# Optimization experiments

Hardware: AMD Instinct MI355X
Metric: run time of the kernel (lower is better)

Reference implementation:

```python
import jax, jax.numpy as jnp
import numpy as np

IN_F = 4096
OUT_F = 4096
N = 16384


def setup_inputs() -> dict:
    key = jax.random.key(0)
    ks = jax.random.split(key, 7)
    return {
        "x": jax.random.normal(ks[0], (N, IN_F), dtype=jnp.float32),
        "weight_mu": jax.random.normal(ks[1], (OUT_F, IN_F), dtype=jnp.float32) * 0.1,
        "weight_rho": jax.random.normal(ks[2], (OUT_F, IN_F), dtype=jnp.float32) * 0.1,
        "bias_mu": jax.random.normal(ks[3], (OUT_F,), dtype=jnp.float32) * 0.1,
        "bias_rho": jax.random.normal(ks[4], (OUT_F,), dtype=jnp.float32) * 0.1,
        "eps_w": jax.random.normal(ks[5], (OUT_F, IN_F), dtype=jnp.float32),
        "eps_b": jax.random.normal(ks[6], (OUT_F,), dtype=jnp.float32),
    }


def reference(x, weight_mu, weight_rho, bias_mu, bias_rho, eps_w, eps_b):
    # softplus: log(1 + exp(rho)), written as log1p(exp(.)) for stability
    weight = weight_mu + jnp.log1p(jnp.exp(weight_rho)) * eps_w  # [out, in]
    bias = bias_mu + jnp.log1p(jnp.exp(bias_rho)) * eps_b        # [out]
    # F.linear(x, W, b) = x @ W.T + b
    return jnp.einsum("ni,oi->no", x, weight) + bias
```

## Files before the change

kernel.cpp:

```cpp
#include <hip/hip_runtime.h>
#include <hip/hip_bf16.h>

typedef unsigned short u16;
typedef __attribute__((ext_vector_type(4))) float f32x4;
typedef __attribute__((ext_vector_type(8))) short bf16x8;

__device__ __forceinline__ u16 f2bf(float f) {
    union { float f; unsigned u; } v; v.f = f;
    unsigned r = (v.u + 0x7fffu + ((v.u >> 16) & 1u)) >> 16;
    return (u16)r;
}

__device__ __forceinline__ float softplus(float x) {
    return (x > 15.f) ? x : log1pf(__expf(x));
}

__device__ __forceinline__ void gload_lds16(const void* g, void* l) {
    __builtin_amdgcn_global_load_lds(
        (__attribute__((address_space(1))) void*)(g),
        (__attribute__((address_space(3))) void*)(l),
        16, 0, 0);
}

#define BAR() do { asm volatile("" ::: "memory"); \
                   __builtin_amdgcn_s_barrier();  \
                   asm volatile("" ::: "memory"); } while (0)

__global__ __launch_bounds__(256) void prep_all(
        const float* __restrict__ x,
        const float* __restrict__ wmu, const float* __restrict__ wrho,
        const float* __restrict__ ew,
        const float* __restrict__ bmu, const float* __restrict__ brho,
        const float* __restrict__ eb,
        u16* __restrict__ xb, u16* __restrict__ wb, float* __restrict__ bs,
        int nx4, int nw4, int nb) {
    int i = blockIdx.x * 256 + threadIdx.x;
    if (i < nx4) {
        float4 v = ((const float4*)x)[i];
        ushort4 o;
        o.x = f2bf(v.x); o.y = f2bf(v.y); o.z = f2bf(v.z); o.w = f2bf(v.w);
        ((ushort4*)xb)[i] = o;
    }
    if (i < nw4) {
        float4 m = ((const float4*)wmu)[i];
        float4 r = ((const float4*)wrho)[i];
        float4 e = ((const float4*)ew)[i];
        ushort4 o;
        o.x = f2bf(m.x + softplus(r.x) * e.x);
        o.y = f2bf(m.y + softplus(r.y) * e.y);
        o.z = f2bf(m.z + softplus(r.z) * e.z);
        o.w = f2bf(m.w + softplus(r.w) * e.w);
        ((ushort4*)wb)[i] = o;
    }
    if (i < nb) {
        bs[i] = bmu[i] + softplus(brho[i]) * eb[i];
    }
}

__device__ __forceinline__ bf16x8 ld_frag(const u16* region, int r0, int ks, int lane) {
    int row = r0 + (lane & 15);
    int kc  = (ks * 4 + (lane >> 4)) ^ (row & 7);
    return *(const bf16x8*)((const char*)region + row * 128 + kc * 16);
}

template <int MB, int NB>
__device__ __forceinline__ void mfma_quad(f32x4 (&acc)[8][4],
                                          const bf16x8 (&av)[4][2],
                                          const bf16x8 (&bv)[2][2]) {
#pragma unroll
    for (int ks = 0; ks < 2; ++ks)
#pragma unroll
        for (int mi = 0; mi < 4; ++mi)
#pragma unroll
            for (int ni = 0; ni < 2; ++ni)
                acc[MB + mi][NB + ni] = __builtin_amdgcn_mfma_f32_16x16x32_bf16(
                    av[mi][ks], bv[ni][ks], acc[MB + mi][NB + ni], 0, 0, 0);
}

#define STAGE(region, h, P, koff) do {                                          \
    gload_lds16(P[h][0] + (koff), (char*)(region) + (h) * 16384 + (w * 2 + 0) * 1024); \
    gload_lds16(P[h][1] + (koff), (char*)(region) + (h) * 16384 + (w * 2 + 1) * 1024); \
} while (0)

#define RD_A(reg, roff)                                                \
    _Pragma("unroll")                                                  \
    for (int mi = 0; mi < 4; ++mi)                                     \
        _Pragma("unroll")                                              \
        for (int ks = 0; ks < 2; ++ks)                                 \
            a[mi][ks] = ld_frag(reg, wr * 128 + (roff) + mi * 16, ks, lane)

#define RD_B(dst, reg, roff)                                           \
    _Pragma("unroll")                                                  \
    for (int ni = 0; ni < 2; ++ni)                                     \
        _Pragma("unroll")                                              \
        for (int ks = 0; ks < 2; ++ks)                                 \
            dst[ni][ks] = ld_frag(reg, wc * 64 + (roff) + ni * 16, ks, lane)

__global__ __launch_bounds__(512, 2) void gemm256_8ph(
        const u16* __restrict__ A,
        const u16* __restrict__ B,
        const float* __restrict__ bias,
        float* __restrict__ C,
        int M, int Nout, int K) {
    __shared__ __attribute__((aligned(16))) u16 smem[4][16384];
    u16* A0 = smem[0]; u16* B0 = smem[1];
    u16* A1 = smem[2]; u16* B1 = smem[3];

    const int tid  = threadIdx.x;
    const int lane = tid & 63;
    const int w    = tid >> 6;
    const int wr   = w >> 2;
    const int wc   = w & 3;

    const int nbn = Nout >> 8;
    const int nwg = (M >> 8) * nbn;
    const int cpx = nwg >> 3;
    const int swz = ((int)blockIdx.x & 7) * cpx + ((int)blockIdx.x >> 3);
    const int m0 = (swz / nbn) << 8;
    const int n0 = (swz % nbn) << 8;

    const u16* PA[2][2]; const u16* PB[2][2];
#pragma unroll
    for (int q = 0; q < 2; ++q) {
        int c   = (w * 2 + q) * 64 + lane;
        int row = c >> 3;
        int kc  = (c & 7) ^ (row & 7);
#pragma unroll
        for (int h = 0; h < 2; ++h) {
            PA[h][q] = A + (size_t)(m0 + h * 128 + row) * K + kc * 8;
            PB[h][q] = B + (size_t)(n0 + h * 128 + row) * K + kc * 8;
        }
    }

    bf16x8 a[4][2], bl[2][2], bh[2][2];
    f32x4 acc[8][4] = {};

    const int NT = K >> 6;
    const int NI = NT >> 1;

    STAGE(B0, 0, PB, 0);  STAGE(B0, 1, PB, 0);
    STAGE(A0, 0, PA, 0);  STAGE(A0, 1, PA, 0);
    STAGE(B1, 0, PB, 64); STAGE(B1, 1, PB, 64);
    asm volatile("s_waitcnt vmcnt(4)" ::: "memory");
    BAR();
    RD_A(A0, 0);

#pragma unroll 1
    for (int i = 0; i < NI; ++i) {
        int t2 = 2 * i + 2; if (t2 >= NT) t2 -= NT;
        int t3 = 2 * i + 3; if (t3 >= NT) t3 -= NT;
        const int k1 = (2 * i + 1) << 6;
        const int k2 = t2 << 6;
        const int k3 = t3 << 6;

        RD_B(bl, B0, 0);
        STAGE(A1, 0, PA, k1);
        BAR();
        asm volatile("s_waitcnt lgkmcnt(0)" ::: "memory");
        __builtin_amdgcn_s_setprio(1);
        mfma_quad<0, 0>(acc, a, bl);
        __builtin_amdgcn_s_setprio(0);
        BAR();

        RD_B(bh, B0, 32);
        STAGE(A1, 1, PA, k1);
        BAR();
        asm volatile("s_waitcnt lgkmcnt(0)" ::: "memory");
        __builtin_amdgcn_s_setprio(1);
        mfma_quad<0, 2>(acc, a, bh);
        __builtin_amdgcn_s_setprio(0);
        BAR();

        RD_A(A0, 64);
        STAGE(B0, 0, PB, k2);
        BAR();
        asm volatile("s_waitcnt lgkmcnt(0)" ::: "memory");
        __builtin_amdgcn_s_setprio(1);
        mfma_quad<4, 2>(acc, a, bh);
        __builtin_amdgcn_s_setprio(0);
        BAR();

        STAGE(B0, 1, PB, k2);
        asm volatile("s_waitcnt vmcnt(4)" ::: "memory");
        BAR();
        __builtin_amdgcn_s_setprio(1);
        mfma_quad<4, 0>(acc, a, bl);
        __builtin_amdgcn_s_setprio(0);
        RD_A(A1, 0);
        BAR();

        RD_B(bl, B1, 0);
        STAGE(A0, 0, PA, k2);
        BAR();
        asm volatile("s_waitcnt lgkmcnt(0)" ::: "memory");
        __builtin_amdgcn_s_setprio(1);
        mfma_quad<0, 0>(acc, a, bl);
        __builtin_amdgcn_s_setprio(0);
        BAR();

        RD_B(bh, B1, 32);
        STAGE(A0, 1, PA, k2);
        BAR();
        asm volatile("s_waitcnt lgkmcnt(0)" ::: "memory");
        __builtin_amdgcn_s_setprio(1);
        mfma_quad<0, 2>(acc, a, bh);
        __builtin_amdgcn_s_setprio(0);
        BAR();

        RD_A(A1, 64);
        STAGE(B1, 0, PB, k3);
        BAR();
        asm volatile("s_waitcnt lgkmcnt(0)" ::: "memory");
        __builtin_amdgcn_s_setprio(1);
        mfma_quad<4, 2>(acc, a, bh);
        __builtin_amdgcn_s_setprio(0);
        BAR();

        STAGE(B1, 1, PB, k3);
        asm volatile("s_waitcnt vmcnt(4)" ::: "memory");
        BAR();
        __builtin_amdgcn_s_setprio(1);
        mfma_quad<4, 0>(acc, a, bl);
        __builtin_amdgcn_s_setprio(0);
        RD_A(A0, 0);
        BAR();
    }

    asm volatile("s_waitcnt vmcnt(0)" ::: "memory");
    BAR();

    float* elds = (float*)((char*)smem + w * 16384);
    const int ccol = lane & 15;
    const int crow = (lane >> 4) * 4;

    float bv[4];
#pragma unroll
    for (int ni = 0; ni < 4; ++ni)
        bv[ni] = bias[n0 + wc * 64 + ni * 16 + ccol];

#pragma unroll
    for (int h = 0; h < 2; ++h) {
#pragma unroll
        for (int mi = 0; mi < 4; ++mi)
#pragma unroll
            for (int ni = 0; ni < 4; ++ni)
#pragma unroll
                for (int q = 0; q < 4; ++q) {
                    int row_l = mi * 16 + crow + q;
                    int cp = (ni * 16 + ccol) ^ crow;
                    elds[row_l * 64 + cp] = acc[h * 4 + mi][ni][q] + bv[ni];
                }
        asm volatile("s_waitcnt lgkmcnt(0)" ::: "memory");
#pragma unroll
        for (int p = 0; p < 16; ++p) {
            int row_l = p * 4 + (lane >> 4);
            int cb = (lane & 15) * 4;
            float4 v = *(const float4*)&elds[row_l * 64 + (cb ^ ((p & 3) << 2))];
            float* Cp = C + (size_t)(m0 + wr * 128 + h * 64 + row_l) * Nout
                          + (n0 + wc * 64 + cb);
            *(float4*)Cp = v;
        }
        asm volatile("s_waitcnt lgkmcnt(0)" ::: "memory");
    }
}

extern "C" void kernel_launch(void* const* d_in, const int* in_sizes, int n_in,
                              void* d_out, int out_size, void* d_ws, size_t ws_size,
                              hipStream_t stream) {
    const float* x    = (const float*)d_in[0];
    const float* wmu  = (const float*)d_in[1];
    const float* wrho = (const float*)d_in[2];
    const float* bmu  = (const float*)d_in[3];
    const float* brho = (const float*)d_in[4];
    const float* ew   = (const float*)d_in[5];
    const float* eb   = (const float*)d_in[6];
    float* out = (float*)d_out;

    const int Nout = in_sizes[3];
    const int K    = in_sizes[1] / Nout;
    const int M    = in_sizes[0] / K;

    u16* xb = (u16*)d_ws;
    u16* wb = xb + (size_t)M * K;
    float* bs = (float*)(wb + (size_t)Nout * K);

    const int nx4 = (M * K) / 4;
    const int nw4 = (Nout * K) / 4;
    prep_all<<<(nx4 + 255) / 256, 256, 0, stream>>>(
        x, wmu, wrho, ew, bmu, brho, eb, xb, wb, bs, nx4, nw4, Nout);

    dim3 grid((M / 256) * (Nout / 256));
    gemm256_8ph<<<grid, 512, 0, stream>>>(xb, wb, bs, out, M, Nout, K);
}
```

Before: 566.1 us.

## Use inline-asm LDS fragment reads with precomputed addresses and direct epilogue stores

Replaces the C++ swizzled LDS fragment loads with inline ds_read_b128 instructions that use precomputed per-lane base addresses and immediate offsets, cutting per-iteration address arithmetic. Adds sched_barrier fences after the lgkmcnt waits so the compiler cannot move instructions across them. The epilogue no longer stages results through LDS for coalesced float4 stores and instead writes scalar floats straight from the accumulators. That saves LDS traffic and barriers at the end but produces uncoalesced, strided global stores.

```diff
diff --git a/kernel.cpp b/kernel.cpp
--- a/kernel.cpp
+++ b/kernel.cpp
@@ -25,6 +25,13 @@
 #define BAR() do { asm volatile("" ::: "memory"); \
                    __builtin_amdgcn_s_barrier();  \
                    asm volatile("" ::: "memory"); } while (0)
+
+#define DSR(dst, base, off) \
+    asm volatile("ds_read_b128 %0, %1 offset:%2" : "=v"(dst) : "v"(base), "i"(off))
+
+#define LGKM0_FENCE() do { \
+    asm volatile("s_waitcnt lgkmcnt(0)" ::: "memory"); \
+    __builtin_amdgcn_sched_barrier(0); } while (0)
 
 __global__ __launch_bounds__(256) void prep_all(
         const float* __restrict__ x,
@@ -57,12 +64,6 @@
     }
 }
 
-__device__ __forceinline__ bf16x8 ld_frag(const u16* region, int r0, int ks, int lane) {
-    int row = r0 + (lane & 15);
-    int kc  = (ks * 4 + (lane >> 4)) ^ (row & 7);
-    return *(const bf16x8*)((const char*)region + row * 128 + kc * 16);
-}
-
 template <int MB, int NB>
 __device__ __forceinline__ void mfma_quad(f32x4 (&acc)[8][4],
                                           const bf16x8 (&av)[4][2],
@@ -82,19 +83,19 @@
     gload_lds16(P[h][1] + (koff), (char*)(region) + (h) * 16384 + (w * 2 + 1) * 1024); \
 } while (0)
 
-#define RD_A(reg, roff)                                                \
-    _Pragma("unroll")                                                  \
-    for (int mi = 0; mi < 4; ++mi)                                     \
-        _Pragma("unroll")                                              \
-        for (int ks = 0; ks < 2; ++ks)                                 \
-            a[mi][ks] = ld_frag(reg, wr * 128 + (roff) + mi * 16, ks, lane)
-
-#define RD_B(dst, reg, roff)                                           \
-    _Pragma("unroll")                                                  \
-    for (int ni = 0; ni < 2; ++ni)                                     \
-        _Pragma("unroll")                                              \
-        for (int ks = 0; ks < 2; ++ks)                                 \
-            dst[ni][ks] = ld_frag(reg, wc * 64 + (roff) + ni * 16, ks, lane)
+#define RD_A(Rbyte, roff) do {                                         \
+    unsigned r0a = aB0 + ((Rbyte) + (roff) * 128);                     \
+    unsigned r1a = aB1 + ((Rbyte) + (roff) * 128);                     \
+    DSR(a[0][0], r0a, 0);    DSR(a[0][1], r1a, 0);                     \
+    DSR(a[1][0], r0a, 2048); DSR(a[1][1], r1a, 2048);                  \
+    DSR(a[2][0], r0a, 4096); DSR(a[2][1], r1a, 4096);                  \
+    DSR(a[3][0], r0a, 6144); DSR(a[3][1], r1a, 6144); } while (0)
+
+#define RD_B(dst, Rbyte, roff) do {                                    \
+    unsigned r0b = bB0 + ((Rbyte) + (roff) * 128);                     \
+    unsigned r1b = bB1 + ((Rbyte) + (roff) * 128);                     \
+    DSR(dst[0][0], r0b, 0);    DSR(dst[0][1], r1b, 0);                 \
+    DSR(dst[1][0], r0b, 2048); DSR(dst[1][1], r1b, 2048); } while (0)
 
 __global__ __launch_bounds__(512, 2) void gemm256_8ph(
         const u16* __restrict__ A,
@@ -103,14 +104,15 @@
         float* __restrict__ C,
         int M, int Nout, int K) {
     __shared__ __attribute__((aligned(16))) u16 smem[4][16384];
-    u16* A0 = smem[0]; u16* B0 = smem[1];
-    u16* A1 = smem[2]; u16* B1 = smem[3];
 
     const int tid  = threadIdx.x;
     const int lane = tid & 63;
     const int w    = tid >> 6;
     const int wr   = w >> 2;
     const int wc   = w & 3;
+
+    u16* A0 = smem[0]; u16* B0 = smem[1];
+    u16* A1 = smem[2]; u16* B1 = smem[3];
 
     const int nbn = Nout >> 8;
     const int nwg = (M >> 8) * nbn;
@@ -132,6 +134,14 @@
         }
     }
 
+    const unsigned sb    = (unsigned)(size_t)(void*)&smem[0][0];
+    const unsigned loff0 = (unsigned)((lane & 15) * 128 + (((lane >> 4) ^ (lane & 7)) & 7) * 16);
+    const unsigned loff1 = (unsigned)((lane & 15) * 128 + ((((lane >> 4) + 4) ^ (lane & 7)) & 7) * 16);
+    const unsigned aB0 = sb + (unsigned)(wr * 128 * 128) + loff0;
+    const unsigned aB1 = sb + (unsigned)(wr * 128 * 128) + loff1;
+    const unsigned bB0 = sb + (unsigned)(wc * 64 * 128) + loff0;
+    const unsigned bB1 = sb + (unsigned)(wc * 64 * 128) + loff1;
+
     bf16x8 a[4][2], bl[2][2], bh[2][2];
     f32x4 acc[8][4] = {};
 
@@ -143,7 +153,7 @@
     STAGE(B1, 0, PB, 64); STAGE(B1, 1, PB, 64);
     asm volatile("s_waitcnt vmcnt(4)" ::: "memory");
     BAR();
-    RD_A(A0, 0);
+    RD_A(0, 0);
 
 #pragma unroll 1
     for (int i = 0; i < NI; ++i) {
@@ -153,28 +163,28 @@
         const int k2 = t2 << 6;
         const int k3 = t3 << 6;
 
-        RD_B(bl, B0, 0);
+        RD_B(bl, 32768, 0);
         STAGE(A1, 0, PA, k1);
         BAR();
-        asm volatile("s_waitcnt lgkmcnt(0)" ::: "memory");
+        LGKM0_FENCE();
         __builtin_amdgcn_s_setprio(1);
         mfma_quad<0, 0>(acc, a, bl);
         __builtin_amdgcn_s_setprio(0);
         BAR();
 
-        RD_B(bh, B0, 32);
+        RD_B(bh, 32768, 32);
         STAGE(A1, 1, PA, k1);
         BAR();
-        asm volatile("s_waitcnt lgkmcnt(0)" ::: "memory");
+        LGKM0_FENCE();
         __builtin_amdgcn_s_setprio(1);
         mfma_quad<0, 2>(acc, a, bh);
         __builtin_amdgcn_s_setprio(0);
         BAR();
 
-        RD_A(A0, 64);
+        RD_A(0, 64);
         STAGE(B0, 0, PB, k2);
         BAR();
-        asm volatile("s_waitcnt lgkmcnt(0)" ::: "memory");
+        LGKM0_FENCE();
         __builtin_amdgcn_s_setprio(1);
         mfma_quad<4, 2>(acc, a, bh);
         __builtin_amdgcn_s_setprio(0);
@@ -186,31 +196,31 @@
         __builtin_amdgcn_s_setprio(1);
         mfma_quad<4, 0>(acc, a, bl);
         __builtin_amdgcn_s_setprio(0);
-        RD_A(A1, 0);
-        BAR();
-
-        RD_B(bl, B1, 0);
+        RD_A(65536, 0);
+        BAR();
+
+        RD_B(bl, 98304, 0);
         STAGE(A0, 0, PA, k2);
         BAR();
-        asm volatile("s_waitcnt lgkmcnt(0)" ::: "memory");
+        LGKM0_FENCE();
         __builtin_amdgcn_s_setprio(1);
         mfma_quad<0, 0>(acc, a, bl);
         __builtin_amdgcn_s_setprio(0);
         BAR();
 
-        RD_B(bh, B1, 32);
+        RD_B(bh, 98304, 32);
         STAGE(A0, 1, PA, k2);
         BAR();
-        asm volatile("s_waitcnt lgkmcnt(0)" ::: "memory");
+        LGKM0_FENCE();
         __builtin_amdgcn_s_setprio(1);
         mfma_quad<0, 2>(acc, a, bh);
         __builtin_amdgcn_s_setprio(0);
         BAR();
 
-        RD_A(A1, 64);
+        RD_A(65536, 64);
         STAGE(B1, 0, PB, k3);
         BAR();
-        asm volatile("s_waitcnt lgkmcnt(0)" ::: "memory");
+        LGKM0_FENCE();
         __builtin_amdgcn_s_setprio(1);
         mfma_quad<4, 2>(acc, a, bh);
         __builtin_amdgcn_s_setprio(0);
@@ -222,45 +232,26 @@
         __builtin_amdgcn_s_setprio(1);
         mfma_quad<4, 0>(acc, a, bl);
         __builtin_amdgcn_s_setprio(0);
-        RD_A(A0, 0);
-        BAR();
-    }
-
-    asm volatile("s_waitcnt vmcnt(0)" ::: "memory");
-    BAR();
-
-    float* elds = (float*)((char*)smem + w * 16384);
+        RD_A(0, 0);
+        BAR();
+    }
+
+    asm volatile("s_waitcnt vmcnt(0) lgkmcnt(0)" ::: "memory");
+
+    const int crow = (lane >> 4) * 4;
     const int ccol = lane & 15;
-    const int crow = (lane >> 4) * 4;
-
-    float bv[4];
-#pragma unroll
-    for (int ni = 0; ni < 4; ++ni)
-        bv[ni] = bias[n0 + wc * 64 + ni * 16 + ccol];
-
-#pragma unroll
-    for (int h = 0; h < 2; ++h) {
-#pragma unroll
-        for (int mi = 0; mi < 4; ++mi)
-#pragma unroll
-            for (int ni = 0; ni < 4; ++ni)
-#pragma unroll
-                for (int q = 0; q < 4; ++q) {
-                    int row_l = mi * 16 + crow + q;
-                    int cp = (ni * 16 + ccol) ^ crow;
-                    elds[row_l * 64 + cp] = acc[h * 4 + mi][ni][q] + bv[ni];
-                }
-        asm volatile("s_waitcnt lgkmcnt(0)" ::: "memory");
-#pragma unroll
-        for (int p = 0; p < 16; ++p) {
-            int row_l = p * 4 + (lane >> 4);
-            int cb = (lane & 15) * 4;
-            float4 v = *(const float4*)&elds[row_l * 64 + (cb ^ ((p & 3) << 2))];
-            float* Cp = C + (size_t)(m0 + wr * 128 + h * 64 + row_l) * Nout
-                          + (n0 + wc * 64 + cb);
-            *(float4*)Cp = v;
+#pragma unroll
+    for (int mi = 0; mi < 8; ++mi) {
+#pragma unroll
+        for (int ni = 0; ni < 4; ++ni) {
+            const int row = m0 + wr * 128 + mi * 16 + crow;
+            const int col = n0 + wc * 64 + ni * 16 + ccol;
+            const float bv = bias[col];
+            float* Cp = C + (size_t)row * Nout + col;
+#pragma unroll
+            for (int q = 0; q < 4; ++q)
+                Cp[(size_t)q * Nout] = acc[mi][ni][q] + bv;
         }
-        asm volatile("s_waitcnt lgkmcnt(0)" ::: "memory");
     }
 }
 
```

Measured after the change: 567.4 us. Within noise of the previous version (+0.2%).
